# Performance work log

Measured on AMD Instinct MI355X. Metric: run time of the kernel, lower is better.

Reference implementation:

```python
import jax, jax.numpy as jnp
from jax import lax
import numpy as np

B, Q, C = 128, 200, 92  # batch, num_queries, num_classes (0 = no-object)


def hungarian(cost):
    """Exact Hungarian assignment (augmenting-path / JV potentials, e-maxx form).
    cost: [n, n]. Returns col_of_row: [n] int32, the column matched to each row.
    Uses 1-based columns/rows internally; index 0 is the sentinel."""
    n = cost.shape[0]
    INF = jnp.asarray(1e9, cost.dtype)

    def solve_row(i, carry):
        u, v, p = carry
        p = p.at[0].set(jnp.int32(i))
        minv = jnp.full(n + 1, INF, cost.dtype)
        way = jnp.zeros(n + 1, jnp.int32)
        used = jnp.zeros(n + 1, bool)
        state = (u, v, p, minv, way, used, jnp.int32(0))

        def cond(s):
            _u, _v, _p, _minv, _way, _used, j0 = s
            return _p[j0] != 0

        def body(s):
            u, v, p, minv, way, used, j0 = s
            used = used.at[j0].set(True)
            i0 = p[j0]
            cur = cost[i0 - 1, :] - u[i0] - v[1:]          # reduced costs of row i0
            cur = jnp.where(used[1:], INF, cur)
            upd = cur < minv[1:]
            minv = minv.at[1:].set(jnp.where(upd, cur, minv[1:]))
            way = way.at[1:].set(jnp.where(upd, j0, way[1:]))
            masked = jnp.where(used[1:], INF, minv[1:])
            j1 = jnp.argmin(masked).astype(jnp.int32) + 1
            delta = masked[j1 - 1]
            zero = jnp.asarray(0, cost.dtype)
            u = u.at[p].add(jnp.where(used, delta, zero))  # u[p[j]] += delta for used j (rows distinct)
            v = jnp.where(used, v - delta, v)
            minv = jnp.where(used, minv, minv - delta)
            return (u, v, p, minv, way, used, j1)

        u, v, p, minv, way, used, j0 = lax.while_loop(cond, body, state)

        def aug_body(s):  # flip matching along the alternating path
            p, j0 = s
            j1 = way[j0]
            return p.at[j0].set(p[j1]), j1

        p, _ = lax.while_loop(lambda s: s[1] != 0, aug_body, (p, j0))
        return (u, v, p)

    u0 = jnp.zeros(n + 1, cost.dtype)
    v0 = jnp.zeros(n + 1, cost.dtype)
    p0 = jnp.zeros(n + 1, jnp.int32)
    _, _, p = lax.fori_loop(1, n + 1, solve_row, (u0, v0, p0))
    # p[j] = row matched to column j (1-based); invert to col per row (0-based)
    col_of_row = jnp.zeros(n, jnp.int32).at[p[1:] - 1].set(jnp.arange(n, dtype=jnp.int32))
    return col_of_row


def cost_matrix(pred_cat, pred_bbox, tar_cat, tar_bbox):
    b, q, c = pred_cat.shape
    log_probs = jax.nn.log_softmax(pred_cat, axis=-1)                  # [B,Qp,C]
    idx = jnp.broadcast_to(tar_cat[:, None, :], (b, q, q))             # [B,Qp,Qt]
    ce = -jnp.take_along_axis(log_probs, idx, axis=2)                  # CE(pred_i, tgt_j)
    d = pred_bbox[:, :, None, :] - tar_bbox[:, None, :, :]             # [B,Qp,Qt,4]
    ad = jnp.abs(d)
    sl1 = jnp.where(ad < 1.0, 0.5 * d * d, ad - 0.5).sum(-1)           # SmoothL1 (beta=1)
    mask = (tar_cat != 0).astype(sl1.dtype)[:, None, :]                # bbox loss only for real objects
    return ce + sl1 * mask                                             # [B,Qp,Qt]


def setup_inputs() -> dict:
    key = jax.random.key(0)
    k1, k2, k3, k4 = jax.random.split(key, 4)
    pred_cat = jax.random.normal(k1, (B, Q, C), dtype=jnp.float32)
    pred_bbox = jax.random.uniform(k2, (B, Q, 4), dtype=jnp.float32)
    tar_cat = jax.random.randint(k3, (B, Q), 0, C, dtype=jnp.int32)
    tar_bbox = jax.random.uniform(k4, (B, Q, 4), dtype=jnp.float32)
    return {"pred_cat": pred_cat, "pred_bbox": pred_bbox, "tar_cat": tar_cat, "tar_bbox": tar_bbox}


def reference(pred_cat, pred_bbox, tar_cat, tar_bbox):
    cost = cost_matrix(pred_cat, pred_bbox, tar_cat, tar_bbox)         # [B,Q,Q]
    col = jax.vmap(hungarian)(lax.stop_gradient(cost))                 # assignment on detached cost
    out = jnp.take_along_axis(cost, col[:, :, None], axis=2)[..., 0]   # [B,Q] per-query matched loss
    return out
```

## Files before the change

### kernel.cpp

```cpp
#include <hip/hip_runtime.h>
#include <math.h>

#define BB 128
#define QQ 200
#define CC 92
#define CMPAD (QQ * QQ + 64)

__global__ void lse_kernel(const float* __restrict__ pc, float* __restrict__ lse) {
    int idx = blockIdx.x * blockDim.x + threadIdx.x;
    if (idx >= BB * QQ) return;
    const float* row = pc + (size_t)idx * CC;
    float m = -INFINITY;
    for (int c = 0; c < CC; ++c) m = fmaxf(m, row[c]);
    float s = 0.f;
    for (int c = 0; c < CC; ++c) s += expf(row[c] - m);
    lse[idx] = m + logf(s);
}

__global__ void cost_kernel(const float* __restrict__ pc,
                            const float* __restrict__ pb,
                            const int*   __restrict__ tc,
                            const float* __restrict__ tb,
                            const float* __restrict__ lse,
                            float* __restrict__ cost) {
    long idx = blockIdx.x * (long)blockDim.x + threadIdx.x;
    if (idx >= (long)BB * QQ * QQ) return;
    int j = (int)(idx % QQ);
    int i = (int)((idx / QQ) % QQ);
    int b = (int)(idx / ((long)QQ * QQ));
    int cls = tc[b * QQ + j];
    float ce = lse[b * QQ + i] - pc[((size_t)(b * QQ + i)) * CC + cls];
    const float* pbb = pb + ((size_t)(b * QQ + i)) * 4;
    const float* tbb = tb + ((size_t)(b * QQ + j)) * 4;
    float sl1 = 0.f;
#pragma unroll
    for (int k = 0; k < 4; ++k) {
        float d = pbb[k] - tbb[k];
        float ad = fabsf(d);
        sl1 += (ad < 1.f) ? 0.5f * d * d : (ad - 0.5f);
    }
    float mask = (cls != 0) ? 1.f : 0.f;
    cost[idx] = ce + sl1 * mask;
}

__device__ __forceinline__ int rdlane_i(int x, int l) { return __builtin_amdgcn_readlane(x, l); }
__device__ __forceinline__ float rdlane_f(float x, int l) {
    return __uint_as_float((unsigned)__builtin_amdgcn_readlane((int)__float_as_uint(x), l));
}

__device__ __forceinline__ float wave_fmin_bcast(float x) {
    float y;
#define DPPSTEP(ctrl) \
    y = __uint_as_float((unsigned)__builtin_amdgcn_update_dpp( \
            (int)__float_as_uint(x), (int)__float_as_uint(x), ctrl, 0xf, 0xf, false)); \
    x = fminf(x, y);
    DPPSTEP(0x111) DPPSTEP(0x112) DPPSTEP(0x114) DPPSTEP(0x118)
    DPPSTEP(0x142) DPPSTEP(0x143)
#undef DPPSTEP
    return rdlane_f(x, 63);
}

__global__ __launch_bounds__(64) void hungarian_kernel(const float* __restrict__ cost,
                                                       float* __restrict__ out) {
    const int b = blockIdx.x;
    const int t = threadIdx.x;
    const float* cb = cost + (size_t)b * QQ * QQ;

    __shared__ __align__(16) float cm[CMPAD];

    {
        const float4* src = (const float4*)cb;
        float4* dst = (float4*)cm;
        for (int idx = t; idx < QQ * QQ / 4; idx += 64) dst[idx] = src[idx];
    }

    const float INF = 1e9f;
    const int nval = (t < 8) ? 4 : 3;

    float v[4]     = {0.f, 0.f, 0.f, 0.f};
    int   pslot[4] = {0, 0, 0, 0};
    unsigned pp    = 0u;
    float uslot[4] = {0.f, 0.f, 0.f, 0.f};
    float minv[4];
    int   waysl[4];
    int   usedm;
    float usent;

    for (int i = 1; i <= QQ; ++i) {
        minv[0] = minv[1] = minv[2] = minv[3] = INF;
        waysl[0] = waysl[1] = waysl[2] = waysl[3] = 0;
        usedm = 0;
        usent = 0.f;
        int j0 = 0;
        float u0 = 0.f;
        const float* crow = cm + (i - 1) * QQ;
        float c0 = crow[t];
        float c1 = crow[64 + t];
        float c2 = crow[128 + t];
        float c3 = crow[192 + t];

        for (;;) {
            if (j0 > 0) {
                int s = (j0 - 1) >> 6;
                if (((j0 - 1) & 63) == t) usedm |= 1 << s;
            }

            float kv0, kv1, kv2, kv3;
            {
                float cur;
                cur = c0 - u0 - v[0];
                if (!(usedm & 1) && cur < minv[0]) { minv[0] = cur; waysl[0] = j0; }
                kv0 = (usedm & 1) ? INF : minv[0];
                cur = c1 - u0 - v[1];
                if (!(usedm & 2) && cur < minv[1]) { minv[1] = cur; waysl[1] = j0; }
                kv1 = (usedm & 2) ? INF : minv[1];
                cur = c2 - u0 - v[2];
                if (!(usedm & 4) && cur < minv[2]) { minv[2] = cur; waysl[2] = j0; }
                kv2 = (usedm & 4) ? INF : minv[2];
                cur = c3 - u0 - v[3];
                if (!(usedm & 8) && t < 8 && cur < minv[3]) { minv[3] = cur; waysl[3] = j0; }
                kv3 = ((usedm & 8) || t >= 8) ? INF : minv[3];
            }

            float gmin = wave_fmin_bcast(fminf(fminf(kv0, kv1), fminf(kv2, kv3)));
            float delta = gmin;

            unsigned long long m0 = __ballot(kv0 == gmin);
            unsigned long long m1 = __ballot(kv1 == gmin);
            unsigned long long m2 = __ballot(kv2 == gmin);
            unsigned long long m3 = __ballot(kv3 == gmin);
            int j1;
            if (m0)      j1 = 1   + (int)__builtin_ctzll(m0);
            else if (m1) j1 = 65  + (int)__builtin_ctzll(m1);
            else if (m2) j1 = 129 + (int)__builtin_ctzll(m2);
            else         j1 = 193 + (int)__builtin_ctzll(m3);

            int kk = (j1 - 1) >> 6, ln = (j1 - 1) & 63;
            float us = (kk == 0) ? uslot[0] : (kk == 1) ? uslot[1]
                      : (kk == 2) ? uslot[2] : uslot[3];
            int pi = (int)(((unsigned)rdlane_i((int)pp, ln) >> (kk * 8)) & 255u);

            int nr = (pi > 0 ? pi : 1) - 1;
            const float* nrow = cm + nr * QQ;
            float n0 = nrow[t];
            float n1 = nrow[64 + t];
            float n2 = nrow[128 + t];
            float n3 = nrow[192 + t];

            float u0n = rdlane_f(us, ln);

#pragma unroll
            for (int k = 0; k < 4; ++k) {
                if (usedm & (1 << k)) {
                    v[k] -= delta;
                    uslot[k] += delta;
                } else if (k < nval) {
                    minv[k] -= delta;
                }
            }
            usent += delta;

            if (pi == 0) { j0 = j1; break; }
            j0 = j1; u0 = u0n;
            c0 = n0; c1 = n1; c2 = n2; c3 = n3;
        }

        {
            int jj = j0;
            while (jj != 0) {
                int jm = jj - 1, km = jm >> 6, lm = jm & 63;
                int ws = (km == 0) ? waysl[0] : (km == 1) ? waysl[1]
                        : (km == 2) ? waysl[2] : waysl[3];
                int jn = rdlane_i(ws, lm);
                int pnew; float unew;
                if (jn == 0) {
                    pnew = i;
                    unew = usent;
                } else {
                    int jm2 = jn - 1, kn = jm2 >> 6, ln2 = jm2 & 63;
                    int   ps2 = (kn == 0) ? pslot[0] : (kn == 1) ? pslot[1]
                               : (kn == 2) ? pslot[2] : pslot[3];
                    float us2 = (kn == 0) ? uslot[0] : (kn == 1) ? uslot[1]
                               : (kn == 2) ? uslot[2] : uslot[3];
                    pnew = rdlane_i(ps2, ln2);
                    unew = rdlane_f(us2, ln2);
                }
                if (lm == t) {
                    pslot[km] = pnew;
                    uslot[km] = unew;
                    int sh = km * 8;
                    pp = (pp & ~(255u << sh)) | ((unsigned)pnew << sh);
                }
                jj = jn;
            }
        }
    }

#pragma unroll
    for (int k = 0; k < 4; ++k) {
        if (k < nval) {
            int jc = 1 + t + 64 * k;
            int row = pslot[k] - 1;
            out[b * QQ + row] = cm[row * QQ + (jc - 1)];
        }
    }
}

extern "C" void kernel_launch(void* const* d_in, const int* in_sizes, int n_in,
                              void* d_out, int out_size, void* d_ws, size_t ws_size,
                              hipStream_t stream) {
    const float* pred_cat  = (const float*)d_in[0];
    const float* pred_bbox = (const float*)d_in[1];
    const int*   tar_cat   = (const int*)d_in[2];
    const float* tar_bbox  = (const float*)d_in[3];
    float* out = (float*)d_out;

    float* cost = (float*)d_ws;
    float* lse  = cost + (size_t)BB * QQ * QQ;

    lse_kernel<<<(BB * QQ + 255) / 256, 256, 0, stream>>>(pred_cat, lse);
    cost_kernel<<<((long)BB * QQ * QQ + 255) / 256, 256, 0, stream>>>(
        pred_cat, pred_bbox, tar_cat, tar_bbox, lse, cost);
    hungarian_kernel<<<BB, 64, 0, stream>>>(cost, out);
}
```

Baseline: 1.377 ms.

## Fuse LSE and cost-matrix computation into the Hungarian kernel

```diff
diff --git a/kernel.cpp b/kernel.cpp
--- a/kernel.cpp
+++ b/kernel.cpp
@@ -5,43 +5,6 @@
 #define QQ 200
 #define CC 92
 #define CMPAD (QQ * QQ + 64)
-
-__global__ void lse_kernel(const float* __restrict__ pc, float* __restrict__ lse) {
-    int idx = blockIdx.x * blockDim.x + threadIdx.x;
-    if (idx >= BB * QQ) return;
-    const float* row = pc + (size_t)idx * CC;
-    float m = -INFINITY;
-    for (int c = 0; c < CC; ++c) m = fmaxf(m, row[c]);
-    float s = 0.f;
-    for (int c = 0; c < CC; ++c) s += expf(row[c] - m);
-    lse[idx] = m + logf(s);
-}
-
-__global__ void cost_kernel(const float* __restrict__ pc,
-                            const float* __restrict__ pb,
-                            const int*   __restrict__ tc,
-                            const float* __restrict__ tb,
-                            const float* __restrict__ lse,
-                            float* __restrict__ cost) {
-    long idx = blockIdx.x * (long)blockDim.x + threadIdx.x;
-    if (idx >= (long)BB * QQ * QQ) return;
-    int j = (int)(idx % QQ);
-    int i = (int)((idx / QQ) % QQ);
-    int b = (int)(idx / ((long)QQ * QQ));
-    int cls = tc[b * QQ + j];
-    float ce = lse[b * QQ + i] - pc[((size_t)(b * QQ + i)) * CC + cls];
-    const float* pbb = pb + ((size_t)(b * QQ + i)) * 4;
-    const float* tbb = tb + ((size_t)(b * QQ + j)) * 4;
-    float sl1 = 0.f;
-#pragma unroll
-    for (int k = 0; k < 4; ++k) {
-        float d = pbb[k] - tbb[k];
-        float ad = fabsf(d);
-        sl1 += (ad < 1.f) ? 0.5f * d * d : (ad - 0.5f);
-    }
-    float mask = (cls != 0) ? 1.f : 0.f;
-    cost[idx] = ce + sl1 * mask;
-}
 
 __device__ __forceinline__ int rdlane_i(int x, int l) { return __builtin_amdgcn_readlane(x, l); }
 __device__ __forceinline__ float rdlane_f(float x, int l) {
@@ -60,22 +23,72 @@
     return rdlane_f(x, 63);
 }
 
-__global__ __launch_bounds__(64) void hungarian_kernel(const float* __restrict__ cost,
-                                                       float* __restrict__ out) {
+__global__ __launch_bounds__(64) void hungarian_fused(const float* __restrict__ pc,
+                                                      const float* __restrict__ pb,
+                                                      const int*   __restrict__ tc,
+                                                      const float* __restrict__ tb,
+                                                      float* __restrict__ out) {
     const int b = blockIdx.x;
     const int t = threadIdx.x;
-    const float* cb = cost + (size_t)b * QQ * QQ;
 
     __shared__ __align__(16) float cm[CMPAD];
-
-    {
-        const float4* src = (const float4*)cb;
-        float4* dst = (float4*)cm;
-        for (int idx = t; idx < QQ * QQ / 4; idx += 64) dst[idx] = src[idx];
-    }
+    __shared__ float lse_s[QQ];
 
     const float INF = 1e9f;
     const int nval = (t < 8) ? 4 : 3;
+
+    int   cls[4];
+    float tbx[4][4];
+#pragma unroll
+    for (int k = 0; k < 4; ++k) {
+        if (k < nval) {
+            int jj = t + 64 * k;
+            cls[k] = tc[b * QQ + jj];
+            const float4 v4 = *reinterpret_cast<const float4*>(tb + ((size_t)(b * QQ + jj)) * 4);
+            tbx[k][0] = v4.x; tbx[k][1] = v4.y; tbx[k][2] = v4.z; tbx[k][3] = v4.w;
+        } else {
+            cls[k] = 0;
+            tbx[k][0] = tbx[k][1] = tbx[k][2] = tbx[k][3] = 0.f;
+        }
+    }
+
+#pragma unroll
+    for (int k = 0; k < 4; ++k) {
+        if (k < nval) {
+            int r = t + 64 * k;
+            const float* row = pc + ((size_t)(b * QQ + r)) * CC;
+            float m = -INFINITY;
+            for (int c = 0; c < CC; ++c) m = fmaxf(m, row[c]);
+            float s = 0.f;
+            for (int c = 0; c < CC; ++c) s += expf(row[c] - m);
+            lse_s[r] = m + logf(s);
+        }
+    }
+    __syncthreads();
+
+#pragma unroll 2
+    for (int i = 0; i < QQ; ++i) {
+        const float4 pb4 = *reinterpret_cast<const float4*>(pb + ((size_t)(b * QQ + i)) * 4);
+        const float pbb[4] = {pb4.x, pb4.y, pb4.z, pb4.w};
+        const float lsei = lse_s[i];
+        const float* pcrow = pc + ((size_t)(b * QQ + i)) * CC;
+#pragma unroll
+        for (int k = 0; k < 4; ++k) {
+            if (k < nval) {
+                float ce = lsei - pcrow[cls[k]];
+                float sl1 = 0.f;
+#pragma unroll
+                for (int d = 0; d < 4; ++d) {
+                    float df = pbb[d] - tbx[k][d];
+                    float ad = fabsf(df);
+                    sl1 += (ad < 1.f) ? 0.5f * df * df : (ad - 0.5f);
+                }
+                float mask = (cls[k] != 0) ? 1.f : 0.f;
+                cm[i * QQ + t + 64 * k] = ce + sl1 * mask;
+            }
+        }
+    }
+    __syncthreads();
 
     float v[4]     = {0.f, 0.f, 0.f, 0.f};
     int   pslot[4] = {0, 0, 0, 0};
@@ -214,12 +227,7 @@
     const int*   tar_cat   = (const int*)d_in[2];
     const float* tar_bbox  = (const float*)d_in[3];
     float* out = (float*)d_out;
-
-    float* cost = (float*)d_ws;
-    float* lse  = cost + (size_t)BB * QQ * QQ;
-
-    lse_kernel<<<(BB * QQ + 255) / 256, 256, 0, stream>>>(pred_cat, lse);
-    cost_kernel<<<((long)BB * QQ * QQ + 255) / 256, 256, 0, stream>>>(
-        pred_cat, pred_bbox, tar_cat, tar_bbox, lse, cost);
-    hungarian_kernel<<<BB, 64, 0, stream>>>(cost, out);
-}
+    (void)d_ws; (void)ws_size;
+
+    hungarian_fused<<<BB, 64, 0, stream>>>(pred_cat, pred_bbox, tar_cat, tar_bbox, out);
+}
```

Result: slower. 1.428 ms (+3.7%).
